# Kernel optimization log

Measured on AMD Instinct MI355X. Metric: run time of the kernel, lower is better.

The kernel has to match this reference:

```python
import jax, jax.numpy as jnp
import numpy as np

N_NODES = 50000
EMBED_DIM = 100
N_RAND_EDGES = 600000
NEG_SLOPE = 0.2  # alpha in the original module


def _build_pairs(n_nodes, n_edges, seed=0):
    """Replicates: neighbors(v) = unique(out_nbrs(v) U in_nbrs(v)) for all v,
    flattened into (seg=v, nbr=u) pair arrays (symmetrized, deduped edge list)."""
    rng = np.random.default_rng(seed)
    src = rng.integers(0, n_nodes, n_edges)
    dst = rng.integers(0, n_nodes, n_edges)
    ring = np.arange(n_nodes)  # guarantee every node has a neighbor
    src = np.concatenate([src, ring])
    dst = np.concatenate([dst, (ring + 1) % n_nodes])
    seg = np.concatenate([src, dst])
    nbr = np.concatenate([dst, src])
    pairs = np.unique(np.stack([seg, nbr], axis=1), axis=0)  # sorted by seg
    return pairs[:, 0].astype(np.int32), pairs[:, 1].astype(np.int32)


def setup_inputs() -> dict:
    key = jax.random.key(0)
    k1, k2 = jax.random.split(key)
    hidden = jax.random.normal(k1, (N_NODES, EMBED_DIM), dtype=jnp.float32)
    # nn.Linear(embed_dim, 1, bias=False) weight, kaiming-uniform-ish scale
    W = jax.random.normal(k2, (EMBED_DIM,), dtype=jnp.float32) / np.sqrt(EMBED_DIM)
    seg_np, nbr_np = _build_pairs(N_NODES, N_RAND_EDGES)
    return {"hidden": hidden, "W": W,
            "seg": jnp.asarray(seg_np), "nbr": jnp.asarray(nbr_np)}


def reference(hidden, W, seg, nbr):
    n = hidden.shape[0]
    h_i = hidden[seg]            # [P, D] center node repeated per neighbor
    h_j = hidden[nbr]            # [P, D] gathered neighbor embeddings
    scores = jnp.einsum('pd,d->p', h_i * h_j, W)           # a(neighbors*hidden)
    scores = jnp.where(scores >= 0, scores, NEG_SLOPE * scores)  # leaky_relu
    # per-node (segment) softmax, numerically stable
    m = jax.ops.segment_max(scores, seg, num_segments=n)
    e = jnp.exp(scores - m[seg])
    z = jax.ops.segment_sum(e, seg, num_segments=n)
    alpha = e / z[seg]                                      # [P]
    out = jax.ops.segment_sum(alpha[:, None] * h_j, seg, num_segments=n)  # [N, D]
    return out
```

## Files before the change

kernel.cpp:

```cpp
#include <hip/hip_runtime.h>
#include <math.h>

#define D 100
#define NEG_SLOPE 0.2f
#define CHUNK 16
#define ROWU 52

typedef _Float16 f16x2 __attribute__((ext_vector_type(2)));
union U32H2 { unsigned int u; f16x2 h; };

__device__ __forceinline__ unsigned int pkh2(float x, float y) {
    U32H2 c; c.h.x = (_Float16)x; c.h.y = (_Float16)y; return c.u;
}
__device__ __forceinline__ float f16lo(unsigned int u) { U32H2 c; c.u = u; return (float)c.h.x; }
__device__ __forceinline__ float f16hi(unsigned int u) { U32H2 c; c.u = u; return (float)c.h.y; }

__device__ __forceinline__ float dot2u(unsigned int au, unsigned int xu, float acc) {
#if __has_builtin(__builtin_amdgcn_fdot2)
    U32H2 a, x; a.u = au; x.u = xu;
    return __builtin_amdgcn_fdot2(a.h, x.h, acc, false);
#else
    return acc + f16lo(au) * f16lo(xu) + f16hi(au) * f16hi(xu);
#endif
}

template<int CTRL>
__device__ __forceinline__ float dppf(float x) {
    return __uint_as_float((unsigned)__builtin_amdgcn_update_dpp(
        0, (int)__float_as_uint(x), CTRL, 0xF, 0xF, true));
}
__device__ __forceinline__ float red16_max(float x) {
    x = fmaxf(x, dppf<0xB1>(x));
    x = fmaxf(x, dppf<0x4E>(x));
    x = fmaxf(x, dppf<0x124>(x));
    x = fmaxf(x, dppf<0x128>(x));
    return x;
}
__device__ __forceinline__ float red16_sum(float x) {
    x += dppf<0xB1>(x);
    x += dppf<0x4E>(x);
    x += dppf<0x124>(x);
    x += dppf<0x128>(x);
    return x;
}

__global__ void prep_kernel(const int* __restrict__ seg,
                            int* __restrict__ row_ptr,
                            const float* __restrict__ hidden,
                            unsigned int* __restrict__ hb,
                            int n, int P, int total25)
{
    int t = blockIdx.x * blockDim.x + threadIdx.x;
    if (t < P) {
        int s0 = seg[t];
        if (t == 0)
            for (int v = 0; v <= s0; v++) row_ptr[v] = 0;
        int s1 = (t + 1 < P) ? seg[t + 1] : n;
        for (int v = s0 + 1; v <= s1; v++) row_ptr[v] = t + 1;
    }
    if (t < total25) {
        int node = t / 25, k = t - node * 25;
        float4 f = ((const float4*)hidden)[t];
        *(uint2*)&hb[node * ROWU + 2 * k] =
            make_uint2(pkh2(f.x, f.y), pkh2(f.z, f.w));
    }
}

__launch_bounds__(256, 8)
__global__ void gat_agg_kernel(const float* __restrict__ hidden,
                               const float* __restrict__ W,
                               const int* __restrict__ nbr,
                               const int* __restrict__ row_ptr,
                               const unsigned int* __restrict__ hb,
                               float* __restrict__ out,
                               int n)
{
    __shared__ __align__(16) unsigned int s_hwp[4][ROWU];
    __shared__ __align__(16) unsigned int s_rows[4][CHUNK][ROWU];
    __shared__ __align__(16) float        s_e[4][CHUNK];

    const int lane = threadIdx.x & 63;
    const int wid  = threadIdx.x >> 6;
    const int v    = blockIdx.x * 4 + wid;
    if (v >= n) return;

    if (lane < 50) {
        float2 h2 = ((const float2*)(hidden + (long)v * D))[lane];
        float2 w2 = ((const float2*)W)[lane];
        s_hwp[wid][lane] = pkh2(h2.x * w2.x, h2.y * w2.y);
    }
    __threadfence_block();

    const int start = row_ptr[v];
    const int end   = row_ptr[v + 1];

    if (end <= start) {
        if (lane < D / 2)
            ((float2*)(out + (long)v * D))[lane] = make_float2(0.f, 0.f);
        return;
    }

    const int q  = lane >> 4;
    const int jl = lane & 15;
    const int t0 = q * 3;

    const uint4* hwq = ((const uint4*)&s_hwp[wid][0]) + t0;
    const uint4 a0 = hwq[0], a1 = hwq[1], a2 = hwq[2];
    uint2 at = make_uint2(0u, 0u);
    if (q == 0) at = *(const uint2*)&s_hwp[wid][48];

    float m = -INFINITY, z = 0.f;
    float accx = 0.f, accy = 0.f;

    for (int c = start; c < end; c += CHUNK) {
        const int  cnt = min(CHUNK, end - c);
        const bool pv  = jl < cnt;

        const int nbv = pv ? nbr[c + jl] : 0;
        const uint4* row16 = ((const uint4*)hb) + nbv * (ROWU / 4) + t0;

        uint4 x0 = row16[0], x1 = row16[1], x2 = row16[2];
        uint2 xt = make_uint2(0u, 0u);
        if (q == 0) xt = *(const uint2*)&hb[nbv * ROWU + 48];

        float p0 = 0.f, p1 = 0.f, p2 = 0.f, p3 = 0.f;
        p0 = dot2u(a0.x, x0.x, p0);  p1 = dot2u(a0.y, x0.y, p1);
        p2 = dot2u(a0.z, x0.z, p2);  p3 = dot2u(a0.w, x0.w, p3);
        p0 = dot2u(a1.x, x1.x, p0);  p1 = dot2u(a1.y, x1.y, p1);
        p2 = dot2u(a1.z, x1.z, p2);  p3 = dot2u(a1.w, x1.w, p3);
        p0 = dot2u(a2.x, x2.x, p0);  p1 = dot2u(a2.y, x2.y, p1);
        p2 = dot2u(a2.z, x2.z, p2);  p3 = dot2u(a2.w, x2.w, p3);
        if (q == 0) {
            p0 = dot2u(at.x, xt.x, p0);
            p1 = dot2u(at.y, xt.y, p1);
        }

        uint4* dst16 = ((uint4*)&s_rows[wid][jl][0]) + t0;
        dst16[0] = x0; dst16[1] = x1; dst16[2] = x2;
        if (q == 0) *(uint2*)&s_rows[wid][jl][48] = xt;

        float part = (p0 + p1) + (p2 + p3);
        part += __shfl_xor(part, 16, 64);
        part += __shfl_xor(part, 32, 64);
        const float s = pv ? (part >= 0.f ? part : NEG_SLOPE * part)
                           : -INFINITY;

        const float m_new = fmaxf(m, red16_max(s));
        const float scale = __expf(m - m_new);
        const float e     = pv ? __expf(s - m_new) : 0.f;
        z = z * scale + red16_sum(e);
        accx *= scale; accy *= scale;

        if (lane < CHUNK) s_e[wid][lane] = e;
        __threadfence_block();

        const int cnt4 = (cnt + 3) & ~3;
        if (lane < D / 2) {
            for (int j0 = 0; j0 < cnt4; j0 += 4) {
                const float4 ev = *(const float4*)&s_e[wid][j0];
                const unsigned int u0 = s_rows[wid][j0    ][lane];
                const unsigned int u1 = s_rows[wid][j0 + 1][lane];
                const unsigned int u2 = s_rows[wid][j0 + 2][lane];
                const unsigned int u3 = s_rows[wid][j0 + 3][lane];
                accx += ev.x * f16lo(u0);  accy += ev.x * f16hi(u0);
                accx += ev.y * f16lo(u1);  accy += ev.y * f16hi(u1);
                accx += ev.z * f16lo(u2);  accy += ev.z * f16hi(u2);
                accx += ev.w * f16lo(u3);  accy += ev.w * f16hi(u3);
            }
        }
        __threadfence_block();
        m = m_new;
    }

    if (lane < D / 2) {
        const float inv = 1.f / z;
        ((float2*)(out + (long)v * D))[lane] = make_float2(accx * inv, accy * inv);
    }
}

extern "C" void kernel_launch(void* const* d_in, const int* in_sizes, int n_in,
                              void* d_out, int out_size, void* d_ws, size_t ws_size,
                              hipStream_t stream) {
    const float* hidden = (const float*)d_in[0];
    const float* W      = (const float*)d_in[1];
    const int*   seg    = (const int*)d_in[2];
    const int*   nbr    = (const int*)d_in[3];
    float*       out    = (float*)d_out;

    const int Ddim = in_sizes[1];
    const int n    = in_sizes[0] / Ddim;
    const int P    = in_sizes[2];

    int* row_ptr = (int*)d_ws;
    size_t hb_off = (((size_t)(n + 1) * 4) + 255) & ~(size_t)255;
    unsigned int* hb = (unsigned int*)((char*)d_ws + hb_off);

    const int total25 = n * 25;
    const int tmax    = (P > total25) ? P : total25;
    hipLaunchKernelGGL(prep_kernel, dim3((tmax + 255) / 256), dim3(256), 0, stream,
                       seg, row_ptr, hidden, hb, n, P, total25);
    hipLaunchKernelGGL(gat_agg_kernel, dim3((n + 3) / 4), dim3(256), 0, stream,
                       hidden, W, nbr, row_ptr, hb, out, n);
}
```

Measured before the change: 128.8 us.

## Process 32 neighbors per chunk with two lanes per neighbor row

```diff
diff --git a/kernel.cpp b/kernel.cpp
--- a/kernel.cpp
+++ b/kernel.cpp
@@ -3,7 +3,7 @@
 
 #define D 100
 #define NEG_SLOPE 0.2f
-#define CHUNK 16
+#define CHUNK 32
 #define ROWU 52
 
 typedef _Float16 f16x2 __attribute__((ext_vector_type(2)));
@@ -12,15 +12,14 @@
 __device__ __forceinline__ unsigned int pkh2(float x, float y) {
     U32H2 c; c.h.x = (_Float16)x; c.h.y = (_Float16)y; return c.u;
 }
-__device__ __forceinline__ float f16lo(unsigned int u) { U32H2 c; c.u = u; return (float)c.h.x; }
-__device__ __forceinline__ float f16hi(unsigned int u) { U32H2 c; c.u = u; return (float)c.h.y; }
 
 __device__ __forceinline__ float dot2u(unsigned int au, unsigned int xu, float acc) {
 #if __has_builtin(__builtin_amdgcn_fdot2)
     U32H2 a, x; a.u = au; x.u = xu;
     return __builtin_amdgcn_fdot2(a.h, x.h, acc, false);
 #else
-    return acc + f16lo(au) * f16lo(xu) + f16hi(au) * f16hi(xu);
+    U32H2 a, x; a.u = au; x.u = xu;
+    return acc + (float)a.h.x * (float)x.h.x + (float)a.h.y * (float)x.h.y;
 #endif
 }
 
@@ -29,18 +28,20 @@
     return __uint_as_float((unsigned)__builtin_amdgcn_update_dpp(
         0, (int)__float_as_uint(x), CTRL, 0xF, 0xF, true));
 }
-__device__ __forceinline__ float red16_max(float x) {
+__device__ __forceinline__ float red32_max(float x) {
     x = fmaxf(x, dppf<0xB1>(x));
     x = fmaxf(x, dppf<0x4E>(x));
     x = fmaxf(x, dppf<0x124>(x));
     x = fmaxf(x, dppf<0x128>(x));
+    x = fmaxf(x, __shfl_xor(x, 16, 64));
     return x;
 }
-__device__ __forceinline__ float red16_sum(float x) {
+__device__ __forceinline__ float red32_sum(float x) {
     x += dppf<0xB1>(x);
     x += dppf<0x4E>(x);
     x += dppf<0x124>(x);
     x += dppf<0x128>(x);
+    x += __shfl_xor(x, 16, 64);
     return x;
 }
 
@@ -66,7 +67,7 @@
     }
 }
 
-__launch_bounds__(256, 8)
+__launch_bounds__(128, 6)
 __global__ void gat_agg_kernel(const float* __restrict__ hidden,
                                const float* __restrict__ W,
                                const int* __restrict__ nbr,
@@ -75,13 +76,13 @@
                                float* __restrict__ out,
                                int n)
 {
-    __shared__ __align__(16) unsigned int s_hwp[4][ROWU];
-    __shared__ __align__(16) unsigned int s_rows[4][CHUNK][ROWU];
-    __shared__ __align__(16) float        s_e[4][CHUNK];
+    __shared__ __align__(16) unsigned int s_hwp[2][ROWU];
+    __shared__ __align__(16) unsigned int s_rows[2][CHUNK][ROWU];
+    __shared__ __align__(16) float        s_e[2][CHUNK];
 
     const int lane = threadIdx.x & 63;
     const int wid  = threadIdx.x >> 6;
-    const int v    = blockIdx.x * 4 + wid;
+    const int v    = blockIdx.x * 2 + wid;
     if (v >= n) return;
 
     if (lane < 50) {
@@ -100,14 +101,11 @@
         return;
     }
 
-    const int q  = lane >> 4;
-    const int jl = lane & 15;
-    const int t0 = q * 3;
-
-    const uint4* hwq = ((const uint4*)&s_hwp[wid][0]) + t0;
-    const uint4 a0 = hwq[0], a1 = hwq[1], a2 = hwq[2];
-    uint2 at = make_uint2(0u, 0u);
-    if (q == 0) at = *(const uint2*)&s_hwp[wid][48];
+    const int h     = lane >> 5;
+    const int jl    = lane & 31;
+    const int ubase = h ? 24 : 0;
+
+    const uint4* hwh = (const uint4*)&s_hwp[wid][ubase];
 
     float m = -INFINITY, z = 0.f;
     float accx = 0.f, accy = 0.f;
@@ -117,11 +115,17 @@
         const bool pv  = jl < cnt;
 
         const int nbv = pv ? nbr[c + jl] : 0;
-        const uint4* row16 = ((const uint4*)hb) + nbv * (ROWU / 4) + t0;
-
-        uint4 x0 = row16[0], x1 = row16[1], x2 = row16[2];
+        const uint4* r16 = (const uint4*)(hb + (size_t)nbv * ROWU + ubase);
+
+        uint4 x0 = r16[0], x1 = r16[1], x2 = r16[2];
+        uint4 x3 = r16[3], x4 = r16[4], x5 = r16[5];
         uint2 xt = make_uint2(0u, 0u);
-        if (q == 0) xt = *(const uint2*)&hb[nbv * ROWU + 48];
+        if (h) xt = *(const uint2*)&hb[(size_t)nbv * ROWU + 48];
+
+        const uint4 a0 = hwh[0], a1 = hwh[1], a2 = hwh[2];
+        const uint4 a3 = hwh[3], a4 = hwh[4], a5 = hwh[5];
+        uint2 at = make_uint2(0u, 0u);
+        if (h) at = *(const uint2*)&s_hwp[wid][48];
 
         float p0 = 0.f, p1 = 0.f, p2 = 0.f, p3 = 0.f;
         p0 = dot2u(a0.x, x0.x, p0);  p1 = dot2u(a0.y, x0.y, p1);
@@ -130,25 +134,31 @@
         p2 = dot2u(a1.z, x1.z, p2);  p3 = dot2u(a1.w, x1.w, p3);
         p0 = dot2u(a2.x, x2.x, p0);  p1 = dot2u(a2.y, x2.y, p1);
         p2 = dot2u(a2.z, x2.z, p2);  p3 = dot2u(a2.w, x2.w, p3);
-        if (q == 0) {
+        p0 = dot2u(a3.x, x3.x, p0);  p1 = dot2u(a3.y, x3.y, p1);
+        p2 = dot2u(a3.z, x3.z, p2);  p3 = dot2u(a3.w, x3.w, p3);
+        p0 = dot2u(a4.x, x4.x, p0);  p1 = dot2u(a4.y, x4.y, p1);
+        p2 = dot2u(a4.z, x4.z, p2);  p3 = dot2u(a4.w, x4.w, p3);
+        p0 = dot2u(a5.x, x5.x, p0);  p1 = dot2u(a5.y, x5.y, p1);
+        p2 = dot2u(a5.z, x5.z, p2);  p3 = dot2u(a5.w, x5.w, p3);
+        if (h) {
             p0 = dot2u(at.x, xt.x, p0);
             p1 = dot2u(at.y, xt.y, p1);
         }
 
-        uint4* dst16 = ((uint4*)&s_rows[wid][jl][0]) + t0;
+        uint4* dst16 = (uint4*)&s_rows[wid][jl][ubase];
         dst16[0] = x0; dst16[1] = x1; dst16[2] = x2;
-        if (q == 0) *(uint2*)&s_rows[wid][jl][48] = xt;
+        dst16[3] = x3; dst16[4] = x4; dst16[5] = x5;
+        if (h) *(uint2*)&s_rows[wid][jl][48] = xt;
 
         float part = (p0 + p1) + (p2 + p3);
-        part += __shfl_xor(part, 16, 64);
         part += __shfl_xor(part, 32, 64);
         const float s = pv ? (part >= 0.f ? part : NEG_SLOPE * part)
                            : -INFINITY;
 
-        const float m_new = fmaxf(m, red16_max(s));
+        const float m_new = fmaxf(m, red32_max(s));
         const float scale = __expf(m - m_new);
         const float e     = pv ? __expf(s - m_new) : 0.f;
-        z = z * scale + red16_sum(e);
+        z = z * scale + red32_sum(e);
         accx *= scale; accy *= scale;
 
         if (lane < CHUNK) s_e[wid][lane] = e;
@@ -158,14 +168,19 @@
         if (lane < D / 2) {
             for (int j0 = 0; j0 < cnt4; j0 += 4) {
                 const float4 ev = *(const float4*)&s_e[wid][j0];
-                const unsigned int u0 = s_rows[wid][j0    ][lane];
-                const unsigned int u1 = s_rows[wid][j0 + 1][lane];
-                const unsigned int u2 = s_rows[wid][j0 + 2][lane];
-                const unsigned int u3 = s_rows[wid][j0 + 3][lane];
-                accx += ev.x * f16lo(u0);  accy += ev.x * f16hi(u0);
-                accx += ev.y * f16lo(u1);  accy += ev.y * f16hi(u1);
-                accx += ev.z * f16lo(u2);  accy += ev.z * f16hi(u2);
-                accx += ev.w * f16lo(u3);  accy += ev.w * f16hi(u3);
+                U32H2 u0, u1, u2, u3;
+                u0.u = s_rows[wid][j0    ][lane];
+                u1.u = s_rows[wid][j0 + 1][lane];
+                u2.u = s_rows[wid][j0 + 2][lane];
+                u3.u = s_rows[wid][j0 + 3][lane];
+                accx = fmaf((float)u0.h.x, ev.x, accx);
+                accy = fmaf((float)u0.h.y, ev.x, accy);
+                accx = fmaf((float)u1.h.x, ev.y, accx);
+                accy = fmaf((float)u1.h.y, ev.y, accy);
+                accx = fmaf((float)u2.h.x, ev.z, accx);
+                accy = fmaf((float)u2.h.y, ev.z, accy);
+                accx = fmaf((float)u3.h.x, ev.w, accx);
+                accy = fmaf((float)u3.h.y, ev.w, accy);
             }
         }
         __threadfence_block();
@@ -199,6 +214,6 @@
     const int tmax    = (P > total25) ? P : total25;
     hipLaunchKernelGGL(prep_kernel, dim3((tmax + 255) / 256), dim3(256), 0, stream,
                        seg, row_ptr, hidden, hb, n, P, total25);
-    hipLaunchKernelGGL(gat_agg_kernel, dim3((n + 3) / 4), dim3(256), 0, stream,
+    hipLaunchKernelGGL(gat_agg_kernel, dim3((n + 1) / 2), dim3(128), 0, stream,
                        hidden, W, nbr, row_ptr, hb, out, n);
 }
```

New measurement: 131.9 us. +2.4%, slower.
